# Kernel tuning notes

Hardware: AMD Instinct MI355X
Metric: run time of the kernel (lower is better)

## Reference

```python
import jax, jax.numpy as jnp
import numpy as np

K_PRESERVED = 384   # num_preserved_tokens
NUM_HEADS = 6       # config.num_attention_heads // 2


def setup_inputs() -> dict:
    key = jax.random.key(0)
    ks = jax.random.split(key, 10)
    B, L, D, H = 16, 512, 768, 12
    U = D // 2  # num_units of the router attention
    s = 0.02
    return {
        "hidden_states": jax.random.normal(ks[0], (B, L, D), jnp.float32),
        "self_attention_scores": jax.random.uniform(ks[1], (B, H, L, L), jnp.float32),
        "Wq": jax.random.normal(ks[2], (D, U), jnp.float32) * s,
        "bq": jnp.zeros((U,), jnp.float32),
        "Wk": jax.random.normal(ks[3], (D, U), jnp.float32) * s,
        "bk": jnp.zeros((U,), jnp.float32),
        "Wv": jax.random.normal(ks[4], (D, U), jnp.float32) * s,
        "bv": jnp.zeros((U,), jnp.float32),
        "Wo": jax.random.normal(ks[5], (U, D), jnp.float32) * s,
        "bo": jnp.zeros((D,), jnp.float32),
    }


def _forward(hidden_states, self_attention_scores, Wq, bq, Wk, bk, Wv, bv, Wo, bo):
    B, L, D = hidden_states.shape
    K = K_PRESERVED
    r = L - K  # number of tokens merged away by ToMe
    batch_idx = jnp.arange(B)[:, None]

    class_token = hidden_states[:, :1, :]

    # importance = column sums of head-averaged attention with zeroed diagonal (detached)
    s = jax.lax.stop_gradient(jnp.mean(self_attention_scores, axis=1))  # [B,L,L]
    s = s * (1.0 - jnp.eye(L, dtype=s.dtype))
    importance = jnp.sum(s, axis=1)  # [B,L]
    _, important_idx = jax.lax.top_k(importance, K)  # [B,K]
    important_mask = jnp.zeros((B, L), bool).at[batch_idx, important_idx].set(True)

    # --- ToMe bipartite_soft_matching(hidden_states, r), mode='mean' ---
    metric = jax.lax.stop_gradient(hidden_states)
    metric = metric / jnp.linalg.norm(metric, axis=-1, keepdims=True)
    a, b = metric[:, ::2, :], metric[:, 1::2, :]            # [B,L/2,D] each
    sim = jnp.einsum('bid,bjd->bij', a, b)                   # [B,L/2,L/2]
    node_max = jnp.max(sim, axis=-1)                         # [B,L/2]
    node_idx = jnp.argmax(sim, axis=-1)                      # [B,L/2]
    edge_idx = jnp.argsort(-node_max, axis=-1)               # descending
    src_idx = edge_idx[:, :r]                                # merged src tokens
    unm_idx = edge_idx[:, r:]                                # unmerged src tokens
    dst_idx = jnp.take_along_axis(node_idx, src_idx, axis=1)  # [B,r]

    src_x = hidden_states[:, ::2, :]
    dst_x = hidden_states[:, 1::2, :]                        # [B,L/2,D]
    unm = jnp.take_along_axis(src_x, unm_idx[..., None], axis=1)   # [B,L/2-r,D]
    src_sel = jnp.take_along_axis(src_x, src_idx[..., None], axis=1)  # [B,r,D]
    # scatter_reduce(mean, include_self=True): (dst + sum srcs) / (1 + count)
    sums = dst_x.at[batch_idx, dst_idx].add(src_sel)
    counts = jnp.ones((B, L // 2), dst_x.dtype).at[batch_idx, dst_idx].add(1.0)
    dst_merged = sums / counts[..., None]
    preserved_tokens = jnp.concatenate([unm, dst_merged], axis=1)  # [B,K,D]

    # attention_mask is None -> sentences is the first token
    sentences = hidden_states[:, :1, :]

    # unpreserved tokens: boolean-mask gather, preserving original order
    order = jnp.argsort(important_mask.astype(jnp.int32), axis=1, stable=True)
    unp_idx = order[:, : L - K]                              # [B,L-K]
    unpreserved = hidden_states[batch_idx, unp_idx]          # [B,L-K,D]

    # router multi-head attention: query=sentence, key/value=unpreserved
    U = Wq.shape[1]
    hd = U // NUM_HEADS
    q = (sentences @ Wq + bq).reshape(B, 1, NUM_HEADS, hd)
    k = (unpreserved @ Wk + bk).reshape(B, L - K, NUM_HEADS, hd)
    v = (unpreserved @ Wv + bv).reshape(B, L - K, NUM_HEADS, hd)
    att = jax.nn.softmax(jnp.einsum('bqhd,bkhd->bhqk', q, k) / jnp.sqrt(jnp.asarray(hd, q.dtype)), axis=-1)
    ctx = jnp.einsum('bhqk,bkhd->bqhd', att, v).reshape(B, 1, U)
    new_token = ctx @ Wo + bo                                # [B,1,D]

    final_token = jnp.concatenate([class_token, preserved_tokens, new_token], axis=1)  # [B,K+2,D]
    return final_token


def reference(hidden_states, self_attention_scores, Wq, bq, Wk, bk, Wv, bv, Wo, bo):
    return _forward(hidden_states, self_attention_scores, Wq, bq, Wk, bk, Wv, bv, Wo, bo)
```

## Files before the change

### kernel.cpp

```cpp
#include <hip/hip_runtime.h>
#include <hip/hip_bf16.h>

#define BB 16
#define LL 512
#define DD 768
#define NHEAD 12
#define HALF 256
#define KPRES 384
#define RCNT 128
#define UDIM 384
#define NH2 6
#define HD 64

__device__ float              g_colsum_part[BB * NHEAD * 4 * LL];
__device__ float              g_norms[BB * LL];
__device__ unsigned long long g_nodep_part[BB * HALF * 4];
__device__ int                g_unm[BB * RCNT];
__device__ int                g_srctok[BB * RCNT];
__device__ int                g_srcdst[BB * RCNT];
__device__ int                g_unp[BB * RCNT];
__device__ float              g_ctx[BB * UDIM];

__global__ void k_colnorm(const float* __restrict__ sc, const float* __restrict__ hs) {
    int blk = blockIdx.x;
    int t = threadIdx.x;
    __shared__ float red[256];
    if (blk < BB * NHEAD * 4) {
        int ic = blk & 3;
        int bh = blk >> 2;
        const float* base = sc + (size_t)bh * LL * LL;
        int i0 = ic * 128;
        float ax = 0.f, ay = 0.f;
        for (int i = 0; i < 128; i++) {
            float2 v = ((const float2*)(base + (size_t)(i0 + i) * LL))[t];
            ax += v.x; ay += v.y;
        }
#pragma unroll
        for (int c = 0; c < 2; c++) {
            int cj = 2 * t + c;
            if (cj >= i0 && cj < i0 + 128) {
                float d = base[(size_t)cj * LL + cj];
                if (c == 0) ax -= d; else ay -= d;
            }
        }
        g_colsum_part[(size_t)blk * LL + 2 * t] = ax;
        g_colsum_part[(size_t)blk * LL + 2 * t + 1] = ay;
    } else {
        int row = blk - BB * NHEAD * 4;
        const float* src = hs + (size_t)row * DD;
        float v0 = src[t], v1 = src[t + 256], v2 = src[t + 512];
        red[t] = ((0.f + v0 * v0) + v1 * v1) + v2 * v2;
        __syncthreads();
        for (int s = 128; s > 0; s >>= 1) {
            if (t < s) red[t] += red[t + s];
            __syncthreads();
        }
        if (t == 0) g_norms[row] = sqrtf(red[0]);
    }
}

__global__ void k_sim(const float* __restrict__ hs) {
    int b = blockIdx.x, it = blockIdx.y, jt = blockIdx.z;
    int i0 = it * 64, j0 = jt * 64;
    __shared__ float As[64][20];
    __shared__ float BsT[16][68];
    __shared__ float nA[64], nB[64];
    __shared__ unsigned long long cand[64][16];
    int t  = threadIdx.x;
    int ti = t >> 4, tj = t & 15;
    if (t < 64) nA[t] = g_norms[b * LL + 2 * (i0 + t)];
    else if (t < 128) nB[t - 64] = g_norms[b * LL + 2 * (j0 + t - 64) + 1];
    float acc[4][4];
#pragma unroll
    for (int a = 0; a < 4; a++)
#pragma unroll
        for (int c = 0; c < 4; c++) acc[a][c] = 0.f;
    const float* hb = hs + (size_t)b * LL * DD;
    int sr = t >> 2, sc4 = t & 3;
    const float* arow = hb + (size_t)(2 * (i0 + sr)) * DD;
    const float* brow = hb + (size_t)(2 * (j0 + sr) + 1) * DD;
    __syncthreads();
    float inA = nA[sr], inB = nB[sr];
    float4 a4 = ((const float4*)arow)[sc4];
    float4 b4 = ((const float4*)brow)[sc4];
    a4.x /= inA; a4.y /= inA; a4.z /= inA; a4.w /= inA;
    b4.x /= inB; b4.y /= inB; b4.z /= inB; b4.w /= inB;
    for (int s = 0; s < 48; s++) {
        __syncthreads();
        *(float4*)&As[sr][4 * sc4] = a4;
        BsT[4 * sc4 + 0][sr] = b4.x;
        BsT[4 * sc4 + 1][sr] = b4.y;
        BsT[4 * sc4 + 2][sr] = b4.z;
        BsT[4 * sc4 + 3][sr] = b4.w;
        __syncthreads();
        if (s + 1 < 48) {
            int d0 = (s + 1) * 16;
            a4 = ((const float4*)(arow + d0))[sc4];
            b4 = ((const float4*)(brow + d0))[sc4];
            a4.x /= inA; a4.y /= inA; a4.z /= inA; a4.w /= inA;
            b4.x /= inB; b4.y /= inB; b4.z /= inB; b4.w /= inB;
        }
#pragma unroll
        for (int c4 = 0; c4 < 4; c4++) {
            float4 av[4], bk4[4];
#pragma unroll
            for (int a = 0; a < 4; a++) av[a] = *(const float4*)&As[ti * 4 + a][4 * c4];
#pragma unroll
            for (int k = 0; k < 4; k++) bk4[k] = *(const float4*)&BsT[4 * c4 + k][4 * tj];
#pragma unroll
            for (int k = 0; k < 4; k++) {
#pragma unroll
                for (int a = 0; a < 4; a++) {
                    float ak = ((const float*)&av[a])[k];
#pragma unroll
                    for (int c = 0; c < 4; c++)
                        acc[a][c] += ak * ((const float*)&bk4[k])[c];
                }
            }
        }
    }
#pragma unroll
    for (int a = 0; a < 4; a++) {
        unsigned long long bp = 0ULL;
#pragma unroll
        for (int c = 0; c < 4; c++) {
            int jg = j0 + tj * 4 + c;
            unsigned u = __float_as_uint(acc[a][c]);
            u = (u & 0x80000000u) ? ~u : (u | 0x80000000u);
            unsigned long long p = ((unsigned long long)u << 32) | (unsigned long long)(255 - jg);
            if (p > bp) bp = p;
        }
        cand[ti * 4 + a][tj] = bp;
    }
    __syncthreads();
    if (t < 64) {
        unsigned long long m = cand[t][0];
#pragma unroll
        for (int c2 = 1; c2 < 16; c2++) { unsigned long long v = cand[t][c2]; if (v > m) m = v; }
        g_nodep_part[((size_t)b * HALF + i0 + t) * 4 + jt] = m;
    }
}

__global__ void k_seledge(int* dummy) {
    int b = blockIdx.x, t = threadIdx.x;
    __shared__ float v[LL];
    __shared__ int pos[LL];
    __shared__ float nm[HALF];
    __shared__ int   ni[HALF];
    float imp = 0.f;
    for (int p = 0; p < NHEAD * 4; p++)
        imp += g_colsum_part[((size_t)b * NHEAD * 4 + p) * LL + t];
    v[t] = imp;
    __syncthreads();
    int cnt = 0;
    for (int k = 0; k < LL; k++) {
        float vk = v[k];
        cnt += (vk > imp) || (vk == imp && k < t);
    }
    int notp = (cnt >= KPRES) ? 1 : 0;
    pos[t] = notp;
    __syncthreads();
    for (int s = 1; s < LL; s <<= 1) {
        int add = (t >= s) ? pos[t - s] : 0;
        __syncthreads();
        pos[t] += add;
        __syncthreads();
    }
    if (notp) g_unp[b * RCNT + pos[t] - 1] = t;
    if (t < HALF) {
        unsigned long long p = g_nodep_part[((size_t)b * HALF + t) * 4 + 0];
#pragma unroll
        for (int q = 1; q < 4; q++) {
            unsigned long long w = g_nodep_part[((size_t)b * HALF + t) * 4 + q];
            if (w > p) p = w;
        }
        unsigned u = (unsigned)(p >> 32);
        unsigned bits = (u & 0x80000000u) ? (u & 0x7FFFFFFFu) : ~u;
        nm[t] = __uint_as_float(bits);
        ni[t] = 255 - (int)(p & 0xFFFFFFFFu);
    }
    __syncthreads();
    if (t < HALF) {
        float vv = nm[t];
        int cnt2 = 0;
        for (int k = 0; k < HALF; k++) {
            float vk = nm[k];
            cnt2 += (vk > vv) || (vk == vv && k < t);
        }
        if (cnt2 < RCNT) {
            g_srctok[b * RCNT + cnt2] = t;
            g_srcdst[b * RCNT + cnt2] = ni[t];
        } else {
            g_unm[b * RCNT + (cnt2 - RCNT)] = 2 * t;
        }
    }
}

__global__ void k_attn(const float* __restrict__ hs,
                       const float* __restrict__ Wq, const float* __restrict__ bq,
                       const float* __restrict__ Wk, const float* __restrict__ bk,
                       const float* __restrict__ Wv, const float* __restrict__ bv) {
    int h = blockIdx.x % NH2, b = blockIdx.x / NH2;
    int t = threadIdx.x;
    __shared__ float h0[DD];
    __shared__ float wk2[DD];
    __shared__ float hbar[DD];
    __shared__ float qs[HD];
    __shared__ float red[256];
    __shared__ float att[RCNT];
    __shared__ int   toks[RCNT];
    __shared__ float qbk;
    const float* hb = hs + (size_t)b * LL * DD;
    for (int d = t; d < DD; d += 256) h0[d] = hb[d];
    if (t < RCNT) toks[t] = g_unp[b * RCNT + t];
    __syncthreads();
    {
        int u = t & 63, part = t >> 6;
        float a = 0.f;
        for (int d = part * 192; d < part * 192 + 192; d++)
            a += h0[d] * Wq[(size_t)d * UDIM + h * HD + u];
        red[t] = a;
        __syncthreads();
        if (t < HD)
            qs[t] = bq[h * HD + t] + red[t] + red[t + 64] + red[t + 128] + red[t + 192];
        __syncthreads();
    }
    for (int d = t; d < DD; d += 256) {
        const float4* wrow = (const float4*)(Wk + (size_t)d * UDIM + h * HD);
        const float4* q4 = (const float4*)qs;
        float4 s4 = {0.f, 0.f, 0.f, 0.f};
#pragma unroll
        for (int u4 = 0; u4 < 16; u4++) {
            float4 w = wrow[u4], q = q4[u4];
            s4.x += q.x * w.x; s4.y += q.y * w.y; s4.z += q.z * w.z; s4.w += q.w * w.w;
        }
        wk2[d] = (s4.x + s4.y) + (s4.z + s4.w);
    }
    if (t == 0) {
        float a = 0.f;
        for (int u = 0; u < HD; u++) a += qs[u] * bk[h * HD + u];
        qbk = a;
    }
    __syncthreads();
    {
        int tok = t >> 1, half = t & 1;
        const float4* hr4 = (const float4*)(hb + (size_t)toks[tok] * DD) + half * 96;
        const float4* wk4 = (const float4*)wk2 + half * 96;
        float4 s4 = {0.f, 0.f, 0.f, 0.f};
        for (int d4 = 0; d4 < 96; d4++) {
            float4 w = wk4[d4], x = hr4[d4];
            s4.x += w.x * x.x; s4.y += w.y * x.y; s4.z += w.z * x.z; s4.w += w.w * x.w;
        }
        red[t] = (s4.x + s4.y) + (s4.z + s4.w);
    }
    __syncthreads();
    float lg = -1e30f;
    if (t < RCNT) lg = (qbk + red[2 * t] + red[2 * t + 1]) * 0.125f;
    __syncthreads();
    red[t] = lg;
    __syncthreads();
    for (int s = 128; s > 0; s >>= 1) {
        if (t < s) red[t] = fmaxf(red[t], red[t + s]);
        __syncthreads();
    }
    float mx = red[0];
    __syncthreads();
    float e = (t < RCNT) ? expf(lg - mx) : 0.f;
    red[t] = e;
    __syncthreads();
    for (int s = 128; s > 0; s >>= 1) {
        if (t < s) red[t] += red[t + s];
        __syncthreads();
    }
    float inv = 1.f / red[0];
    __syncthreads();
    if (t < RCNT) att[t] = e * inv;
    __syncthreads();
    if (t < DD / 4) {
        float4 a4 = {0.f, 0.f, 0.f, 0.f};
        for (int s2 = 0; s2 < RCNT; s2++) {
            float w = att[s2];
            float4 x = ((const float4*)(hb + (size_t)toks[s2] * DD))[t];
            a4.x += w * x.x; a4.y += w * x.y; a4.z += w * x.z; a4.w += w * x.w;
        }
        *(float4*)&hbar[4 * t] = a4;
    }
    __syncthreads();
    {
        int u = t & 63, part = t >> 6;
        float a = 0.f;
        for (int d = part * 192; d < part * 192 + 192; d++)
            a += hbar[d] * Wv[(size_t)d * UDIM + h * HD + u];
        red[t] = a;
        __syncthreads();
        if (t < HD)
            g_ctx[b * UDIM + h * HD + t] =
                bv[h * HD + t] + red[t] + red[t + 64] + red[t + 128] + red[t + 192];
    }
}

__global__ void k_rows(const float* __restrict__ hs,
                       const float* __restrict__ Wo, const float* __restrict__ bo,
                       float* __restrict__ out) {
    int blk = blockIdx.x;
    int t = threadIdx.x;
    if (blk < BB * 385) {
        int row = blk % 385, b = blk / 385;
        float4* o4 = (float4*)(out + ((size_t)b * 386 + row) * DD);
        if (row == 0) {
            const float4* s4 = (const float4*)(hs + (size_t)b * LL * DD);
            o4[t] = s4[t];
        } else if (row <= RCNT) {
            int tok = g_unm[b * RCNT + row - 1];
            const float4* s4 = (const float4*)(hs + ((size_t)b * LL + tok) * DD);
            o4[t] = s4[t];
        } else {
            int j = row - 1 - RCNT;
            __shared__ int ss[RCNT], sd[RCNT];
            if (t < RCNT) { ss[t] = g_srctok[b * RCNT + t]; sd[t] = g_srcdst[b * RCNT + t]; }
            __syncthreads();
            float4 acc = ((const float4*)(hs + ((size_t)b * LL + 2 * j + 1) * DD))[t];
            float cnt = 1.f;
            for (int s2 = 0; s2 < RCNT; s2++) {
                if (sd[s2] == j) {
                    float4 v = ((const float4*)(hs + ((size_t)b * LL + 2 * ss[s2]) * DD))[t];
                    acc.x += v.x; acc.y += v.y; acc.z += v.z; acc.w += v.w;
                    cnt += 1.f;
                }
            }
            float4 r; r.x = acc.x / cnt; r.y = acc.y / cnt; r.z = acc.z / cnt; r.w = acc.w / cnt;
            o4[t] = r;
        }
    } else {
        int b = blk - BB * 385;
        __shared__ float c[UDIM];
        c[t] = g_ctx[b * UDIM + t];
        c[t + 192] = g_ctx[b * UDIM + t + 192];
        __syncthreads();
#pragma unroll
        for (int kk = 0; kk < 4; kk++) {
            int dd = t + 192 * kk;
            float acc = bo[dd];
            for (int u = 0; u < UDIM; u++)
                acc += c[u] * Wo[(size_t)u * DD + dd];
            out[((size_t)b * 386 + 385) * DD + dd] = acc;
        }
    }
}

extern "C" void kernel_launch(void* const* d_in, const int* in_sizes, int n_in,
                              void* d_out, int out_size, void* d_ws, size_t ws_size,
                              hipStream_t stream) {
    const float* hs = (const float*)d_in[0];
    const float* sc = (const float*)d_in[1];
    const float* Wq = (const float*)d_in[2];
    const float* bq = (const float*)d_in[3];
    const float* Wk = (const float*)d_in[4];
    const float* bk = (const float*)d_in[5];
    const float* Wv = (const float*)d_in[6];
    const float* bv = (const float*)d_in[7];
    const float* Wo = (const float*)d_in[8];
    const float* bo = (const float*)d_in[9];
    float* out = (float*)d_out;
    (void)d_ws; (void)ws_size;

    k_colnorm<<<BB * NHEAD * 4 + BB * LL, 256, 0, stream>>>(sc, hs);
    k_sim<<<dim3(BB, 4, 4), 256, 0, stream>>>(hs);
    k_seledge<<<BB, 512, 0, stream>>>(nullptr);
    k_attn<<<BB * NH2, 256, 0, stream>>>(hs, Wq, bq, Wk, bk, Wv, bv);
    k_rows<<<BB * 385 + BB, 192, 0, stream>>>(hs, Wo, bo, out);
}
```

Before: 523.5 us.

## Fuse launches: norms into sim kernel, attention into row-gather kernel

```diff
diff --git a/kernel.cpp b/kernel.cpp
--- a/kernel.cpp
+++ b/kernel.cpp
@@ -1,5 +1,4 @@
 #include <hip/hip_runtime.h>
-#include <hip/hip_bf16.h>
 
 #define BB 16
 #define LL 512
@@ -13,73 +12,86 @@
 #define HD 64
 
 __device__ float              g_colsum_part[BB * NHEAD * 4 * LL];
-__device__ float              g_norms[BB * LL];
 __device__ unsigned long long g_nodep_part[BB * HALF * 4];
-__device__ int                g_unm[BB * RCNT];
-__device__ int                g_srctok[BB * RCNT];
-__device__ int                g_srcdst[BB * RCNT];
-__device__ int                g_unp[BB * RCNT];
-__device__ float              g_ctx[BB * UDIM];
-
-__global__ void k_colnorm(const float* __restrict__ sc, const float* __restrict__ hs) {
+__device__ int g_unm[BB * RCNT];
+__device__ int g_srctok[BB * RCNT];
+__device__ int g_srcdst[BB * RCNT];
+__device__ int g_unp[BB * RCNT];
+
+__global__ void k_main(const float* __restrict__ sc, const float* __restrict__ hs) {
+    __shared__ __align__(16) float As[64][20];
+    __shared__ __align__(16) float BsT[16][68];
+    __shared__ float nA[64], nB[64];
+    __shared__ unsigned long long cand[64][16];
+    __shared__ float red[256];
+    __shared__ __align__(16) float4 smc[256];
     int blk = blockIdx.x;
     int t = threadIdx.x;
-    __shared__ float red[256];
-    if (blk < BB * NHEAD * 4) {
-        int ic = blk & 3;
-        int bh = blk >> 2;
+
+    if (blk >= 256) {
+        int cb = blk - 256;
+        int ic = cb & 3;
+        int bh = cb >> 2;
         const float* base = sc + (size_t)bh * LL * LL;
         int i0 = ic * 128;
-        float ax = 0.f, ay = 0.f;
-        for (int i = 0; i < 128; i++) {
-            float2 v = ((const float2*)(base + (size_t)(i0 + i) * LL))[t];
-            ax += v.x; ay += v.y;
-        }
-#pragma unroll
-        for (int c = 0; c < 2; c++) {
-            int cj = 2 * t + c;
-            if (cj >= i0 && cj < i0 + 128) {
+        int p = t >> 7;
+        int s = t & 127;
+        float4 acc = {0.f, 0.f, 0.f, 0.f};
+#pragma unroll 8
+        for (int i = 0; i < 64; i++) {
+            float4 v = ((const float4*)(base + (size_t)(i0 + 2 * i + p) * LL))[s];
+            acc.x += v.x; acc.y += v.y; acc.z += v.z; acc.w += v.w;
+        }
+#pragma unroll
+        for (int c = 0; c < 4; c++) {
+            int cj = 4 * s + c;
+            if (cj >= i0 && cj < i0 + 128 && (cj & 1) == p) {
                 float d = base[(size_t)cj * LL + cj];
-                if (c == 0) ax -= d; else ay -= d;
-            }
-        }
-        g_colsum_part[(size_t)blk * LL + 2 * t] = ax;
-        g_colsum_part[(size_t)blk * LL + 2 * t + 1] = ay;
-    } else {
-        int row = blk - BB * NHEAD * 4;
-        const float* src = hs + (size_t)row * DD;
-        float v0 = src[t], v1 = src[t + 256], v2 = src[t + 512];
-        red[t] = ((0.f + v0 * v0) + v1 * v1) + v2 * v2;
-        __syncthreads();
-        for (int s = 128; s > 0; s >>= 1) {
-            if (t < s) red[t] += red[t + s];
-            __syncthreads();
-        }
-        if (t == 0) g_norms[row] = sqrtf(red[0]);
-    }
-}
-
-__global__ void k_sim(const float* __restrict__ hs) {
-    int b = blockIdx.x, it = blockIdx.y, jt = blockIdx.z;
+                if (c == 0) acc.x -= d; else if (c == 1) acc.y -= d;
+                else if (c == 2) acc.z -= d; else acc.w -= d;
+            }
+        }
+        smc[t] = acc;
+        __syncthreads();
+        if (t < 128) {
+            float4 e = smc[t], o = smc[t + 128];
+            float4 r;
+            r.x = e.x + o.x; r.y = e.y + o.y; r.z = e.z + o.z; r.w = e.w + o.w;
+            ((float4*)(g_colsum_part + (size_t)cb * LL))[t] = r;
+        }
+        return;
+    }
+
+    int b = blk >> 4, it = (blk >> 2) & 3, jt = blk & 3;
     int i0 = it * 64, j0 = jt * 64;
-    __shared__ float As[64][20];
-    __shared__ float BsT[16][68];
-    __shared__ float nA[64], nB[64];
-    __shared__ unsigned long long cand[64][16];
-    int t  = threadIdx.x;
+    const float* hb = hs + (size_t)b * LL * DD;
+    {
+        int rl = t >> 1, hf = t & 1;
+        int grow = (rl < 64) ? 2 * (i0 + rl) : 2 * (j0 + rl - 64) + 1;
+        const float4* rp = (const float4*)(hb + (size_t)grow * DD) + hf * 96;
+        float4 ac = {0.f, 0.f, 0.f, 0.f};
+#pragma unroll 4
+        for (int q = 0; q < 96; q++) {
+            float4 v = rp[q];
+            ac.x += v.x * v.x; ac.y += v.y * v.y; ac.z += v.z * v.z; ac.w += v.w * v.w;
+        }
+        red[t] = (ac.x + ac.y) + (ac.z + ac.w);
+        __syncthreads();
+        if (t < 128) {
+            float nrm = sqrtf(red[2 * t] + red[2 * t + 1]);
+            if (t < 64) nA[t] = nrm; else nB[t - 64] = nrm;
+        }
+        __syncthreads();
+    }
     int ti = t >> 4, tj = t & 15;
-    if (t < 64) nA[t] = g_norms[b * LL + 2 * (i0 + t)];
-    else if (t < 128) nB[t - 64] = g_norms[b * LL + 2 * (j0 + t - 64) + 1];
     float acc[4][4];
 #pragma unroll
     for (int a = 0; a < 4; a++)
 #pragma unroll
         for (int c = 0; c < 4; c++) acc[a][c] = 0.f;
-    const float* hb = hs + (size_t)b * LL * DD;
     int sr = t >> 2, sc4 = t & 3;
     const float* arow = hb + (size_t)(2 * (i0 + sr)) * DD;
     const float* brow = hb + (size_t)(2 * (j0 + sr) + 1) * DD;
-    __syncthreads();
     float inA = nA[sr], inB = nB[sr];
     float4 a4 = ((const float4*)arow)[sc4];
     float4 b4 = ((const float4*)brow)[sc4];
@@ -127,8 +139,8 @@
             int jg = j0 + tj * 4 + c;
             unsigned u = __float_as_uint(acc[a][c]);
             u = (u & 0x80000000u) ? ~u : (u | 0x80000000u);
-            unsigned long long p = ((unsigned long long)u << 32) | (unsigned long long)(255 - jg);
-            if (p > bp) bp = p;
+            unsigned long long pk = ((unsigned long long)u << 32) | (unsigned long long)(255 - jg);
+            if (pk > bp) bp = pk;
         }
         cand[ti * 4 + a][tj] = bp;
     }
@@ -141,7 +153,7 @@
     }
 }
 
-__global__ void k_seledge(int* dummy) {
+__global__ void k_seledge() {
     int b = blockIdx.x, t = threadIdx.x;
     __shared__ float v[LL];
     __shared__ int pos[LL];
@@ -196,129 +208,154 @@
     }
 }
 
-__global__ void k_attn(const float* __restrict__ hs,
+__global__ void k_tail(const float* __restrict__ hs,
                        const float* __restrict__ Wq, const float* __restrict__ bq,
                        const float* __restrict__ Wk, const float* __restrict__ bk,
-                       const float* __restrict__ Wv, const float* __restrict__ bv) {
-    int h = blockIdx.x % NH2, b = blockIdx.x / NH2;
-    int t = threadIdx.x;
-    __shared__ float h0[DD];
-    __shared__ float wk2[DD];
-    __shared__ float hbar[DD];
-    __shared__ float qs[HD];
-    __shared__ float red[256];
-    __shared__ float att[RCNT];
-    __shared__ int   toks[RCNT];
-    __shared__ float qbk;
-    const float* hb = hs + (size_t)b * LL * DD;
-    for (int d = t; d < DD; d += 256) h0[d] = hb[d];
-    if (t < RCNT) toks[t] = g_unp[b * RCNT + t];
-    __syncthreads();
-    {
-        int u = t & 63, part = t >> 6;
-        float a = 0.f;
-        for (int d = part * 192; d < part * 192 + 192; d++)
-            a += h0[d] * Wq[(size_t)d * UDIM + h * HD + u];
-        red[t] = a;
-        __syncthreads();
-        if (t < HD)
-            qs[t] = bq[h * HD + t] + red[t] + red[t + 64] + red[t + 128] + red[t + 192];
-        __syncthreads();
-    }
-    for (int d = t; d < DD; d += 256) {
-        const float4* wrow = (const float4*)(Wk + (size_t)d * UDIM + h * HD);
-        const float4* q4 = (const float4*)qs;
-        float4 s4 = {0.f, 0.f, 0.f, 0.f};
-#pragma unroll
-        for (int u4 = 0; u4 < 16; u4++) {
-            float4 w = wrow[u4], q = q4[u4];
-            s4.x += q.x * w.x; s4.y += q.y * w.y; s4.z += q.z * w.z; s4.w += q.w * w.w;
-        }
-        wk2[d] = (s4.x + s4.y) + (s4.z + s4.w);
-    }
-    if (t == 0) {
-        float a = 0.f;
-        for (int u = 0; u < HD; u++) a += qs[u] * bk[h * HD + u];
-        qbk = a;
-    }
-    __syncthreads();
-    {
-        int tok = t >> 1, half = t & 1;
-        const float4* hr4 = (const float4*)(hb + (size_t)toks[tok] * DD) + half * 96;
-        const float4* wk4 = (const float4*)wk2 + half * 96;
-        float4 s4 = {0.f, 0.f, 0.f, 0.f};
-        for (int d4 = 0; d4 < 96; d4++) {
-            float4 w = wk4[d4], x = hr4[d4];
-            s4.x += w.x * x.x; s4.y += w.y * x.y; s4.z += w.z * x.z; s4.w += w.w * x.w;
-        }
-        red[t] = (s4.x + s4.y) + (s4.z + s4.w);
-    }
-    __syncthreads();
-    float lg = -1e30f;
-    if (t < RCNT) lg = (qbk + red[2 * t] + red[2 * t + 1]) * 0.125f;
-    __syncthreads();
-    red[t] = lg;
-    __syncthreads();
-    for (int s = 128; s > 0; s >>= 1) {
-        if (t < s) red[t] = fmaxf(red[t], red[t + s]);
-        __syncthreads();
-    }
-    float mx = red[0];
-    __syncthreads();
-    float e = (t < RCNT) ? expf(lg - mx) : 0.f;
-    red[t] = e;
-    __syncthreads();
-    for (int s = 128; s > 0; s >>= 1) {
-        if (t < s) red[t] += red[t + s];
-        __syncthreads();
-    }
-    float inv = 1.f / red[0];
-    __syncthreads();
-    if (t < RCNT) att[t] = e * inv;
-    __syncthreads();
-    if (t < DD / 4) {
-        float4 a4 = {0.f, 0.f, 0.f, 0.f};
-        for (int s2 = 0; s2 < RCNT; s2++) {
-            float w = att[s2];
-            float4 x = ((const float4*)(hb + (size_t)toks[s2] * DD))[t];
-            a4.x += w * x.x; a4.y += w * x.y; a4.z += w * x.z; a4.w += w * x.w;
-        }
-        *(float4*)&hbar[4 * t] = a4;
-    }
-    __syncthreads();
-    {
-        int u = t & 63, part = t >> 6;
-        float a = 0.f;
-        for (int d = part * 192; d < part * 192 + 192; d++)
-            a += hbar[d] * Wv[(size_t)d * UDIM + h * HD + u];
-        red[t] = a;
-        __syncthreads();
-        if (t < HD)
-            g_ctx[b * UDIM + h * HD + t] =
-                bv[h * HD + t] + red[t] + red[t + 64] + red[t + 128] + red[t + 192];
-    }
-}
-
-__global__ void k_rows(const float* __restrict__ hs,
+                       const float* __restrict__ Wv, const float* __restrict__ bv,
                        const float* __restrict__ Wo, const float* __restrict__ bo,
                        float* __restrict__ out) {
     int blk = blockIdx.x;
     int t = threadIdx.x;
-    if (blk < BB * 385) {
-        int row = blk % 385, b = blk / 385;
-        float4* o4 = (float4*)(out + ((size_t)b * 386 + row) * DD);
-        if (row == 0) {
+    __shared__ float h0[DD];
+    __shared__ __align__(16) float qs[UDIM];
+    __shared__ float qbk6[NH2];
+    __shared__ int   toks[RCNT];
+    __shared__ float red[256];
+    __shared__ float att[NH2][RCNT];
+    __shared__ __align__(16) float buf6[NH2][DD];
+    __shared__ float ctxS[UDIM];
+    __shared__ float pm[4];
+    __shared__ int ss[RCNT], sd[RCNT];
+
+    if (blk < BB) {
+        int b = blk;
+        const float* hb = hs + (size_t)b * LL * DD;
+        for (int d = t; d < DD; d += 256) h0[d] = hb[d];
+        if (t < RCNT) toks[t] = g_unp[b * RCNT + t];
+        __syncthreads();
+        for (int hh = 0; hh < NH2; hh++) {
+            int u = t & 63, part = t >> 6;
+            float a = 0.f;
+            for (int d = part * 192; d < part * 192 + 192; d++)
+                a += h0[d] * Wq[(size_t)d * UDIM + hh * HD + u];
+            red[t] = a;
+            __syncthreads();
+            if (t < HD)
+                qs[hh * HD + t] = bq[hh * HD + t] + red[t] + red[t + 64] + red[t + 128] + red[t + 192];
+            __syncthreads();
+        }
+        for (int hh = 0; hh < NH2; hh++) {
+            for (int d = t; d < DD; d += 256) {
+                const float4* wrow = (const float4*)(Wk + (size_t)d * UDIM + hh * HD);
+                const float4* q4 = (const float4*)(qs + hh * HD);
+                float4 s4 = {0.f, 0.f, 0.f, 0.f};
+#pragma unroll
+                for (int u4 = 0; u4 < 16; u4++) {
+                    float4 w = wrow[u4], q = q4[u4];
+                    s4.x += q.x * w.x; s4.y += q.y * w.y; s4.z += q.z * w.z; s4.w += q.w * w.w;
+                }
+                buf6[hh][d] = (s4.x + s4.y) + (s4.z + s4.w);
+            }
+        }
+        if (t < NH2) {
+            float a = 0.f;
+            for (int u = 0; u < HD; u++) a += qs[t * HD + u] * bk[t * HD + u];
+            qbk6[t] = a;
+        }
+        __syncthreads();
+        for (int hh = 0; hh < NH2; hh++) {
+            int tok = t >> 1, half = t & 1;
+            const float4* hr4 = (const float4*)(hb + (size_t)toks[tok] * DD) + half * 96;
+            const float4* wk4 = (const float4*)(&buf6[hh][0]) + half * 96;
+            float4 s4 = {0.f, 0.f, 0.f, 0.f};
+            for (int d4 = 0; d4 < 96; d4++) {
+                float4 w = wk4[d4], x = hr4[d4];
+                s4.x += w.x * x.x; s4.y += w.y * x.y; s4.z += w.z * x.z; s4.w += w.w * x.w;
+            }
+            red[t] = (s4.x + s4.y) + (s4.z + s4.w);
+            __syncthreads();
+            if (t < RCNT)
+                att[hh][t] = (qbk6[hh] + red[2 * t] + red[2 * t + 1]) * 0.125f;
+            __syncthreads();
+        }
+        for (int hh = 0; hh < NH2; hh++) {
+            float lg = (t < RCNT) ? att[hh][t] : -1e30f;
+            float m = lg;
+#pragma unroll
+            for (int off = 32; off >= 1; off >>= 1) m = fmaxf(m, __shfl_xor(m, off, 64));
+            if ((t & 63) == 0) pm[t >> 6] = m;
+            __syncthreads();
+            float mx = fmaxf(pm[0], pm[1]);
+            float e = (t < RCNT) ? expf(lg - mx) : 0.f;
+            float sume = e;
+#pragma unroll
+            for (int off = 32; off >= 1; off >>= 1) sume += __shfl_xor(sume, off, 64);
+            __syncthreads();
+            if ((t & 63) == 0) pm[t >> 6] = sume;
+            __syncthreads();
+            float inv = 1.f / (pm[0] + pm[1]);
+            if (t < RCNT) att[hh][t] = e * inv;
+            __syncthreads();
+        }
+        if (t < DD / 4) {
+            float4 a[NH2];
+#pragma unroll
+            for (int hh = 0; hh < NH2; hh++) a[hh] = make_float4(0.f, 0.f, 0.f, 0.f);
+            for (int s2 = 0; s2 < RCNT; s2++) {
+                float4 x = ((const float4*)(hb + (size_t)toks[s2] * DD))[t];
+#pragma unroll
+                for (int hh = 0; hh < NH2; hh++) {
+                    float w = att[hh][s2];
+                    a[hh].x += w * x.x; a[hh].y += w * x.y; a[hh].z += w * x.z; a[hh].w += w * x.w;
+                }
+            }
+#pragma unroll
+            for (int hh = 0; hh < NH2; hh++) *(float4*)&buf6[hh][4 * t] = a[hh];
+        }
+        __syncthreads();
+        for (int hh = 0; hh < NH2; hh++) {
+            int u = t & 63, part = t >> 6;
+            float a = 0.f;
+            for (int d = part * 192; d < part * 192 + 192; d++)
+                a += buf6[hh][d] * Wv[(size_t)d * UDIM + hh * HD + u];
+            red[t] = a;
+            __syncthreads();
+            if (t < HD)
+                ctxS[hh * HD + t] = bv[hh * HD + t] + red[t] + red[t + 64] + red[t + 128] + red[t + 192];
+            __syncthreads();
+        }
+        if (t < 192) {
+#pragma unroll
+            for (int kk = 0; kk < 4; kk++) {
+                int dd = t + 192 * kk;
+                float acc = bo[dd];
+                for (int u = 0; u < UDIM; u++)
+                    acc += ctxS[u] * Wo[(size_t)u * DD + dd];
+                out[((size_t)b * 386 + 385) * DD + dd] = acc;
+            }
+        }
+        return;
+    }
+
+    int rblk = blk - BB;
+    int row = rblk % 385, b = rblk / 385;
+    float4* o4 = (float4*)(out + ((size_t)b * 386 + row) * DD);
+    if (row == 0) {
+        if (t < 192) {
             const float4* s4 = (const float4*)(hs + (size_t)b * LL * DD);
             o4[t] = s4[t];
-        } else if (row <= RCNT) {
-            int tok = g_unm[b * RCNT + row - 1];
+        }
+    } else if (row <= RCNT) {
+        int tok = g_unm[b * RCNT + row - 1];
+        if (t < 192) {
             const float4* s4 = (const float4*)(hs + ((size_t)b * LL + tok) * DD);
             o4[t] = s4[t];
-        } else {
-            int j = row - 1 - RCNT;
-            __shared__ int ss[RCNT], sd[RCNT];
-            if (t < RCNT) { ss[t] = g_srctok[b * RCNT + t]; sd[t] = g_srcdst[b * RCNT + t]; }
-            __syncthreads();
+        }
+    } else {
+        int j = row - 1 - RCNT;
+        if (t < RCNT) { ss[t] = g_srctok[b * RCNT + t]; sd[t] = g_srcdst[b * RCNT + t]; }
+        __syncthreads();
+        if (t < 192) {
             float4 acc = ((const float4*)(hs + ((size_t)b * LL + 2 * j + 1) * DD))[t];
             float cnt = 1.f;
             for (int s2 = 0; s2 < RCNT; s2++) {
@@ -328,22 +365,9 @@
                     cnt += 1.f;
                 }
             }
-            float4 r; r.x = acc.x / cnt; r.y = acc.y / cnt; r.z = acc.z / cnt; r.w = acc.w / cnt;
+            float4 r;
+            r.x = acc.x / cnt; r.y = acc.y / cnt; r.z = acc.z / cnt; r.w = acc.w / cnt;
             o4[t] = r;
-        }
-    } else {
-        int b = blk - BB * 385;
-        __shared__ float c[UDIM];
-        c[t] = g_ctx[b * UDIM + t];
-        c[t + 192] = g_ctx[b * UDIM + t + 192];
-        __syncthreads();
-#pragma unroll
-        for (int kk = 0; kk < 4; kk++) {
-            int dd = t + 192 * kk;
-            float acc = bo[dd];
-            for (int u = 0; u < UDIM; u++)
-                acc += c[u] * Wo[(size_t)u * DD + dd];
-            out[((size_t)b * 386 + 385) * DD + dd] = acc;
         }
     }
 }
@@ -364,9 +388,7 @@
     float* out = (float*)d_out;
     (void)d_ws; (void)ws_size;
 
-    k_colnorm<<<BB * NHEAD * 4 + BB * LL, 256, 0, stream>>>(sc, hs);
-    k_sim<<<dim3(BB, 4, 4), 256, 0, stream>>>(hs);
-    k_seledge<<<BB, 512, 0, stream>>>(nullptr);
-    k_attn<<<BB * NH2, 256, 0, stream>>>(hs, Wq, bq, Wk, bk, Wv, bv);
-    k_rows<<<BB * 385 + BB, 192, 0, stream>>>(hs, Wo, bo, out);
+    k_main<<<256 + BB * NHEAD * 4, 256, 0, stream>>>(sc, hs);
+    k_seledge<<<BB, 512, 0, stream>>>();
+    k_tail<<<BB + BB * 385, 256, 0, stream>>>(hs, Wq, bq, Wk, bk, Wv, bv, Wo, bo, out);
 }
```

Result: slower. 754.1 us (+44.0%).
